# Kernel tuning notes

Measured on AMD Instinct MI355X. Metric: run time of the kernel, lower is better.

Reference implementation:

```python
import jax, jax.numpy as jnp
import numpy as np

N, E, D, R, H = 50000, 200000, 128, 4, 64

def setup_inputs() -> dict:
    key = jax.random.key(0)
    ks = jax.random.split(key, 12)
    s = 0.02
    return {
        'node_feature': jax.random.normal(ks[0], (N, D), dtype=jnp.float32),
        'edge_src': jax.random.randint(ks[1], (E,), 0, N, dtype=jnp.int32),
        'edge_dst': jax.random.randint(ks[2], (E,), 0, N, dtype=jnp.int32),
        'edge_type': jax.random.randint(ks[3], (E,), 0, R, dtype=jnp.int32),
        'Wr1': s * jax.random.normal(ks[4], (R, D, H), dtype=jnp.float32),
        'br1': jnp.zeros((R, H), dtype=jnp.float32),
        'Wr2': s * jax.random.normal(ks[5], (R, H, H), dtype=jnp.float32),
        'br2': jnp.zeros((R, H), dtype=jnp.float32),
        'Wr3': s * jax.random.normal(ks[6], (R, H, D), dtype=jnp.float32),
        'br3': jnp.zeros((R, D), dtype=jnp.float32),
        'Wn1': s * jax.random.normal(ks[7], ((R + 1) * D, H), dtype=jnp.float32),
        'bn1': jnp.zeros((H,), dtype=jnp.float32),
        'Wn2': s * jax.random.normal(ks[8], (H, H), dtype=jnp.float32),
        'bn2': jnp.zeros((H,), dtype=jnp.float32),
        'Wn3': s * jax.random.normal(ks[9], (H, D), dtype=jnp.float32),
        'bn3': jnp.zeros((D,), dtype=jnp.float32),
    }

def reference(node_feature, edge_src, edge_dst, edge_type,
              Wr1, br1, Wr2, br2, Wr3, br3,
              Wn1, bn1, Wn2, bn2, Wn3, bn3):
    n, d = node_feature.shape
    r = Wr1.shape[0]
    # gather source node features per edge  [E, D]
    x_src = node_feature[edge_src]
    # per-relation message MLP over all edges (masked below): relu hidden layers,
    # linear output, then outer relu as in message_function
    h = jax.nn.relu(jnp.einsum('ed,rdh->reh', x_src, Wr1) + br1[:, None, :])
    h = jax.nn.relu(jnp.einsum('reh,rhk->rek', h, Wr2) + br2[:, None, :])
    msg = jax.nn.relu(jnp.einsum('rek,rkd->red', h, Wr3) + br3[:, None, :])  # [R, E, D]
    # zero out edges not of this relation type (mirrors boolean masking)
    mask = (edge_type[None, :] == jnp.arange(r, dtype=edge_type.dtype)[:, None])
    msg = msg * mask[:, :, None].astype(msg.dtype)
    # scatter-sum messages into destination node slots  [R, N, D]
    agg = jax.vmap(lambda m: jax.ops.segment_sum(m, edge_dst, num_segments=n))(msg)
    # node_enc_input: [relu(node_feature), agg_0, ..., agg_{R-1}]  -> [N, (R+1)*D]
    node_in = jnp.concatenate(
        [jax.nn.relu(node_feature), agg.transpose(1, 0, 2).reshape(n, r * d)], axis=1)
    # node updater MLP
    h = jax.nn.relu(node_in @ Wn1 + bn1)
    h = jax.nn.relu(h @ Wn2 + bn2)
    return h @ Wn3 + bn3
```

## Files before the change

kernel.cpp:

```cpp
#include <hip/hip_runtime.h>

#define DD 128
#define HH 64
#define RR 4
#define NT 256
#define NNT 512
#define DGRID 512
#define DPART 128

typedef __attribute__((ext_vector_type(8))) __bf16 bf16x8;
typedef __attribute__((ext_vector_type(4))) __bf16 bf16x4;
typedef __attribute__((ext_vector_type(4))) float f32x4;

#define SK128 136
#define SK64  72
#define ABLK  2176

#define O_W1  0
#define O_W2  8704
#define O_W3  13312
#define O_WP  22528
#define O_ACT 31232
#define DSMEM_ELEMS 39936
#define N_W1  0
#define N_W2  8704
#define N_W3  13312
#define N_ACT 22528
#define NSMEM_ELEMS 39936

#define W1T_OFF 0
#define W2T_OFF 32768
#define W3T_OFF 49152
#define WPT_OFF 81920
#define WN1_OFF 114688
#define WN2_OFF 122880
#define WN3_OFF 126976
#define WT_TOTAL 135168

#define MFMA(a, b, c) __builtin_amdgcn_mfma_f32_16x16x32_bf16(a, b, c, 0, 0, 0)


template<int ROWS, int COLS, int STRIDE, int BLK>
__device__ __forceinline__ void stageRM(const __bf16* __restrict__ g, __bf16* s, int tid) {
    constexpr int CH = COLS / 8;
    constexpr int TOT = ROWS * CH;
    #pragma unroll
    for (int i = tid; i < TOT; i += BLK) {
        const int row = i / CH, c8 = i % CH;
        *(bf16x8*)(s + row * STRIDE + c8 * 8) = *(const bf16x8*)(g + row * COLS + c8 * 8);
    }
}

__global__ void k_prep_hist(const float* __restrict__ Wr1, const float* __restrict__ Wr2,
                            const float* __restrict__ Wr3, const float* __restrict__ Wn1,
                            const float* __restrict__ Wn2, const float* __restrict__ Wn3,
                            __bf16* __restrict__ wt,
                            const int* __restrict__ ed, int* __restrict__ dstCnt, int E) {
    int i = blockIdx.x * blockDim.x + threadIdx.x;
    if (i < E) atomicAdd(&dstCnt[ed[i]], 1);
    if (i < 32768) {
        int r = i >> 13, k = (i >> 6) & 127, n = i & 63;
        wt[W1T_OFF + r * 8192 + n * 128 + k] = (__bf16)Wr1[i];
    } else if (i < 49152) {
        int j = i - 32768; int r = j >> 12, k = (j >> 6) & 63, n = j & 63;
        wt[W2T_OFF + r * 4096 + n * 64 + k] = (__bf16)Wr2[j];
    } else if (i < 81920) {
        int j = i - 49152; int r = j >> 13, k = (j >> 7) & 63, n = j & 127;
        wt[W3T_OFF + r * 8192 + n * 64 + k] = (__bf16)Wr3[j];
    } else if (i < 122880) {
        int j = i - 81920; int row = j >> 6, n = j & 63;
        int s = row >> 7, k = row & 127;
        float v = Wn1[j];
        if (s == 0) wt[WN1_OFF + n * 128 + k] = (__bf16)v;
        else        wt[WPT_OFF + (s - 1) * 8192 + n * 128 + k] = (__bf16)v;
    } else if (i < 126976) {
        int j = i - 122880; int k = j >> 6, n = j & 63;
        wt[WN2_OFF + n * 64 + k] = (__bf16)Wn2[j];
    } else if (i < WT_TOTAL) {
        int j = i - 126976; int k = j >> 7, n = j & 127;
        wt[WN3_OFF + n * 64 + k] = (__bf16)Wn3[j];
    }
}

__global__ void k_bsum(const int* __restrict__ dstCnt, int* __restrict__ blkSum, int Nn) {
    int b = blockIdx.x, t = threadIdx.x;
    int g = b * 1024 + t * 4;
    int s = 0;
    if (g + 3 < Nn) { int4 v = *(const int4*)(dstCnt + g); s = v.x + v.y + v.z + v.w; }
    else { for (int k = 0; k < 4; k++) if (g + k < Nn) s += dstCnt[g + k]; }
    for (int off = 32; off > 0; off >>= 1) s += __shfl_down(s, off);
    __shared__ int ws[4];
    if ((t & 63) == 0) ws[t >> 6] = s;
    __syncthreads();
    if (t == 0) blkSum[b] = ws[0] + ws[1] + ws[2] + ws[3];
}

__global__ void k_mid(const int* __restrict__ blkSum, int* __restrict__ blkOff,
                      int* __restrict__ rowStart, int NB, int Nn, int E) {
    int lane = threadIdx.x;
    int s = (lane < NB) ? blkSum[lane] : 0;
    int sc = s;
    #pragma unroll
    for (int off = 1; off < 64; off <<= 1) { int u = __shfl_up(sc, off); if (lane >= off) sc += u; }
    if (lane < NB) blkOff[lane] = sc - s;
    if (lane == 0) rowStart[Nn] = E;
}

__global__ void k_wout(const int* __restrict__ dstCnt, const int* __restrict__ blkOff,
                       int* __restrict__ rowStart, int* __restrict__ dstCursor, int Nn) {
    int b = blockIdx.x, t = threadIdx.x;
    int g = b * 1024 + t * 4;
    int4 v = {0, 0, 0, 0};
    bool full = (g + 3 < Nn);
    if (full) v = *(const int4*)(dstCnt + g);
    else {
        if (g     < Nn) v.x = dstCnt[g];
        if (g + 1 < Nn) v.y = dstCnt[g + 1];
        if (g + 2 < Nn) v.z = dstCnt[g + 2];
    }
    int s = v.x + v.y + v.z + v.w;
    int lane = t & 63, wv = t >> 6;
    int sc = s;
    #pragma unroll
    for (int off = 1; off < 64; off <<= 1) { int u = __shfl_up(sc, off); if (lane >= off) sc += u; }
    __shared__ int wsum[4];
    if (lane == 63) wsum[wv] = sc;
    __syncthreads();
    int wadd = 0;
    for (int i = 0; i < wv; i++) wadd += wsum[i];
    int e0 = blkOff[b] + wadd + sc - s;
    int4 rs; rs.x = e0; rs.y = e0 + v.x; rs.z = rs.y + v.y; rs.w = rs.z + v.z;
    if (full) { *(int4*)(rowStart + g) = rs; *(int4*)(dstCursor + g) = rs; }
    else {
        int a[4] = {rs.x, rs.y, rs.z, rs.w};
        for (int k = 0; k < 4; k++) if (g + k < Nn) { rowStart[g + k] = a[k]; dstCursor[g + k] = a[k]; }
    }
}

__global__ void k_place(const int* __restrict__ et, const int* __restrict__ ed,
                        const int* __restrict__ es, int* __restrict__ dstCursor,
                        int* __restrict__ csrKey, int E, int Nn) {
    int i = blockIdx.x * blockDim.x + threadIdx.x;
    if (i < E) {
        int sl = atomicAdd(&dstCursor[ed[i]], 1);
        csrKey[sl] = et[i] * Nn + es[i];
    }
}

__global__ __launch_bounds__(NT, 2) void k_dense(
    const float* __restrict__ nf,
    const float* __restrict__ br1, const float* __restrict__ br2, const float* __restrict__ br3,
    const __bf16* __restrict__ wt, __bf16* __restrict__ ca, int Nn)
{
    extern __shared__ __bf16 smem[];
    const int r    = blockIdx.x & 3;
    const int part = blockIdx.x >> 2;
    const int tid  = threadIdx.x;
    const int w = tid >> 6;
    const int lane = tid & 63;
    const int ln = lane & 15, qd = lane >> 4;
    const int m0 = w << 4;
    __bf16* act = smem + O_ACT + w * ABLK;

    stageRM<64, 128, SK128, NT>(wt + W1T_OFF + r * 8192, smem + O_W1, tid);
    stageRM<64,  64, SK64 , NT>(wt + W2T_OFF + r * 4096, smem + O_W2, tid);
    stageRM<128, 64, SK64 , NT>(wt + W3T_OFF + r * 8192, smem + O_W3, tid);
    stageRM<64, 128, SK128, NT>(wt + WPT_OFF + r * 8192, smem + O_WP, tid);

    float bv1[4], bv2[4], bv3[8];
    #pragma unroll
    for (int nt = 0; nt < 4; nt++) {
        bv1[nt] = br1[r * HH + nt * 16 + ln];
        bv2[nt] = br2[r * HH + nt * 16 + ln];
    }
    #pragma unroll
    for (int nt = 0; nt < 8; nt++) bv3[nt] = br3[r * DD + nt * 16 + ln];

    const int T = (Nn + 63) >> 6;
    const int mx = tid >> 2, qx = tid & 3;
    __bf16* xr = act + (mx & 15) * SK128 + 32 * qx;

    float4 xv[8];
    int t = part;
    if (t < T) {
        const int node = min(t * 64 + mx, Nn - 1);
        const float4* rp = (const float4*)(nf + (size_t)node * DD) + 8 * qx;
        #pragma unroll
        for (int j = 0; j < 8; j++) xv[j] = rp[j];
    }
    __syncthreads();

    for (; t < T; t += DPART) {
        const int nb0 = t * 64;

        #pragma unroll
        for (int jj = 0; jj < 4; jj++) {
            float4 v0 = xv[2 * jj], v1 = xv[2 * jj + 1];
            bf16x8 p;
            p[0] = (__bf16)v0.x; p[1] = (__bf16)v0.y; p[2] = (__bf16)v0.z; p[3] = (__bf16)v0.w;
            p[4] = (__bf16)v1.x; p[5] = (__bf16)v1.y; p[6] = (__bf16)v1.z; p[7] = (__bf16)v1.w;
            *(bf16x8*)(xr + 8 * jj) = p;
        }
        bf16x8 ax[4];
        #pragma unroll
        for (int i = 0; i < 4; i++)
            ax[i] = *(const bf16x8*)(act + ln * SK128 + i * 32 + 8 * qd);

        const int tn = t + DPART;
        if (tn < T) {
            const int node = min(tn * 64 + mx, Nn - 1);
            const float4* rp = (const float4*)(nf + (size_t)node * DD) + 8 * qx;
            #pragma unroll
            for (int j = 0; j < 8; j++) xv[j] = rp[j];
        }

        {
            f32x4 c[4] = {};
            #pragma unroll
            for (int kk = 0; kk < 4; kk++)
                #pragma unroll
                for (int nt = 0; nt < 4; nt++) {
                    bf16x8 b = *(const bf16x8*)(smem + O_W1 + (nt * 16 + ln) * SK128 + kk * 32 + 8 * qd);
                    c[nt] = MFMA(ax[kk], b, c[nt]);
                }
            #pragma unroll
            for (int nt = 0; nt < 4; nt++)
                #pragma unroll
                for (int rg = 0; rg < 4; rg++) {
                    float v = c[nt][rg] + bv1[nt];
                    act[(qd * 4 + rg) * SK64 + nt * 16 + ln] = (__bf16)fmaxf(v, 0.f);
                }
        }
        {
            bf16x8 a0 = *(const bf16x8*)(act + ln * SK64 + 0 + 8 * qd);
            bf16x8 a1 = *(const bf16x8*)(act + ln * SK64 + 32 + 8 * qd);
            f32x4 c[4] = {};
            #pragma unroll
            for (int nt = 0; nt < 4; nt++) {
                bf16x8 b0 = *(const bf16x8*)(smem + O_W2 + (nt * 16 + ln) * SK64 + 0 + 8 * qd);
                bf16x8 b1 = *(const bf16x8*)(smem + O_W2 + (nt * 16 + ln) * SK64 + 32 + 8 * qd);
                c[nt] = MFMA(a0, b0, c[nt]);
                c[nt] = MFMA(a1, b1, c[nt]);
            }
            #pragma unroll
            for (int nt = 0; nt < 4; nt++)
                #pragma unroll
                for (int rg = 0; rg < 4; rg++) {
                    float v = c[nt][rg] + bv2[nt];
                    act[(qd * 4 + rg) * SK64 + nt * 16 + ln] = (__bf16)fmaxf(v, 0.f);
                }
        }
        {
            bf16x8 a0 = *(const bf16x8*)(act + ln * SK64 + 0 + 8 * qd);
            bf16x8 a1 = *(const bf16x8*)(act + ln * SK64 + 32 + 8 * qd);
            f32x4 c[8];
            #pragma unroll
            for (int nt = 0; nt < 8; nt++) {
                bf16x8 b0 = *(const bf16x8*)(smem + O_W3 + (nt * 16 + ln) * SK64 + 0 + 8 * qd);
                bf16x8 b1 = *(const bf16x8*)(smem + O_W3 + (nt * 16 + ln) * SK64 + 32 + 8 * qd);
                f32x4 acc = {};
                acc = MFMA(a0, b0, acc);
                acc = MFMA(a1, b1, acc);
                c[nt] = acc;
            }
            #pragma unroll
            for (int nt = 0; nt < 8; nt++)
                #pragma unroll
                for (int rg = 0; rg < 4; rg++) {
                    float v = c[nt][rg] + bv3[nt];
                    act[(qd * 4 + rg) * SK128 + nt * 16 + ln] = (__bf16)fmaxf(v, 0.f);
                }
        }
        {
            bf16x8 am[4];
            #pragma unroll
            for (int i = 0; i < 4; i++)
                am[i] = *(const bf16x8*)(act + ln * SK128 + i * 32 + 8 * qd);
            f32x4 c[4] = {};
            #pragma unroll
            for (int kk = 0; kk < 4; kk++)
                #pragma unroll
                for (int nt = 0; nt < 4; nt++) {
                    bf16x8 b = *(const bf16x8*)(smem + O_WP + (nt * 16 + ln) * SK128 + kk * 32 + 8 * qd);
                    c[nt] = MFMA(am[kk], b, c[nt]);
                }
            #pragma unroll
            for (int rg = 0; rg < 4; rg++) {
                const int node = nb0 + m0 + qd * 4 + rg;
                if (node < Nn) {
                    bf16x4 v;
                    v[0] = (__bf16)c[0][rg]; v[1] = (__bf16)c[1][rg];
                    v[2] = (__bf16)c[2][rg]; v[3] = (__bf16)c[3][rg];
                    *(bf16x4*)(ca + ((size_t)r * Nn + node) * HH + ln * 4) = v;
                }
            }
        }
    }
}

__global__ __launch_bounds__(NNT, 4) void k_node(
    const float* __restrict__ nf,
    const float* __restrict__ bn1, const float* __restrict__ bn2, const float* __restrict__ bn3,
    const __bf16* __restrict__ wt, const __bf16* __restrict__ ca,
    const int* __restrict__ rowStart, const int* __restrict__ csrKey,
    float* __restrict__ out, int Nn)
{
    extern __shared__ __bf16 smem[];
    const int nb0 = blockIdx.x * 128;
    const int tid = threadIdx.x;
    const int w = tid >> 6;
    const int lane = tid & 63;
    const int ln = lane & 15, qd = lane >> 4;
    const int m0 = w << 4;
    __bf16* act = smem + N_ACT + w * ABLK;

    stageRM<64, 128, SK128, NNT>(wt + WN1_OFF, smem + N_W1, tid);
    stageRM<64,  64, SK64 , NNT>(wt + WN2_OFF, smem + N_W2, tid);
    stageRM<128, 64, SK64 , NNT>(wt + WN3_OFF, smem + N_W3, tid);
    {
        const int m = tid >> 2, q = tid & 3;
        const int node = min(nb0 + m, Nn - 1);
        const float4* rp = (const float4*)(nf + (size_t)node * DD) + 8 * q;
        __bf16* xr = act + (m & 15) * SK128 + 32 * q;
        #pragma unroll
        for (int jj = 0; jj < 4; jj++) {
            float4 v0 = rp[2 * jj], v1 = rp[2 * jj + 1];
            bf16x8 p;
            p[0] = (__bf16)fmaxf(v0.x, 0.f); p[1] = (__bf16)fmaxf(v0.y, 0.f);
            p[2] = (__bf16)fmaxf(v0.z, 0.f); p[3] = (__bf16)fmaxf(v0.w, 0.f);
            p[4] = (__bf16)fmaxf(v1.x, 0.f); p[5] = (__bf16)fmaxf(v1.y, 0.f);
            p[6] = (__bf16)fmaxf(v1.z, 0.f); p[7] = (__bf16)fmaxf(v1.w, 0.f);
            *(bf16x8*)(xr + 8 * jj) = p;
        }
    }
    bf16x8 ax[4];
    #pragma unroll
    for (int i = 0; i < 4; i++)
        ax[i] = *(const bf16x8*)(act + ln * SK128 + i * 32 + 8 * qd);

    float bv1[4], bv2[4], bv3[8];
    #pragma unroll
    for (int nt = 0; nt < 4; nt++) { bv1[nt] = bn1[nt * 16 + ln]; bv2[nt] = bn2[nt * 16 + ln]; }
    #pragma unroll
    for (int nt = 0; nt < 8; nt++) bv3[nt] = bn3[nt * 16 + ln];

    float agg[4][4] = {};
    {
        const int base = nb0 + m0 + qd * 4;
        int rs[5];
        #pragma unroll
        for (int j = 0; j < 5; j++) rs[j] = rowStart[min(base + j, Nn)];
        int cur[4];
        #pragma unroll
        for (int rg = 0; rg < 4; rg++) cur[rg] = rs[rg];
        const __bf16* cab = ca + ln * 4;

        while (true) {
            int k0[4], k1[4];
            bool v0[4], v1[4];
            bool any = false;
            #pragma unroll
            for (int rg = 0; rg < 4; rg++) {
                const int c0 = cur[rg], e1 = rs[rg + 1];
                v0[rg] = c0 < e1;
                v1[rg] = c0 + 1 < e1;
                if (v0[rg]) k0[rg] = csrKey[c0];
                if (v1[rg]) k1[rg] = csrKey[c0 + 1];
                cur[rg] = c0 + (v0[rg] ? 1 : 0) + (v1[rg] ? 1 : 0);
                any |= v0[rg];
            }
            if (!any) break;
            #pragma unroll
            for (int rg = 0; rg < 4; rg++) {
                if (v0[rg]) {
                    const bf16x4 x = *(const bf16x4*)(cab + (size_t)k0[rg] * HH);
                    agg[rg][0] += (float)x[0]; agg[rg][1] += (float)x[1];
                    agg[rg][2] += (float)x[2]; agg[rg][3] += (float)x[3];
                }
                if (v1[rg]) {
                    const bf16x4 x = *(const bf16x4*)(cab + (size_t)k1[rg] * HH);
                    agg[rg][0] += (float)x[0]; agg[rg][1] += (float)x[1];
                    agg[rg][2] += (float)x[2]; agg[rg][3] += (float)x[3];
                }
            }
        }
    }
    __syncthreads();

    {
        f32x4 c[4] = {};
        #pragma unroll
        for (int kk = 0; kk < 4; kk++)
            #pragma unroll
            for (int nt = 0; nt < 4; nt++) {
                bf16x8 b = *(const bf16x8*)(smem + N_W1 + (nt * 16 + ln) * SK128 + kk * 32 + 8 * qd);
                c[nt] = MFMA(ax[kk], b, c[nt]);
            }
        #pragma unroll
        for (int nt = 0; nt < 4; nt++)
            #pragma unroll
            for (int rg = 0; rg < 4; rg++) {
                float v = c[nt][rg] + bv1[nt] + agg[rg][nt];
                act[(qd * 4 + rg) * SK64 + nt * 16 + ln] = (__bf16)fmaxf(v, 0.f);
            }
    }
    {
        bf16x8 a0 = *(const bf16x8*)(act + ln * SK64 + 0 + 8 * qd);
        bf16x8 a1 = *(const bf16x8*)(act + ln * SK64 + 32 + 8 * qd);
        f32x4 c[4] = {};
        #pragma unroll
        for (int nt = 0; nt < 4; nt++) {
            bf16x8 b0 = *(const bf16x8*)(smem + N_W2 + (nt * 16 + ln) * SK64 + 0 + 8 * qd);
            bf16x8 b1 = *(const bf16x8*)(smem + N_W2 + (nt * 16 + ln) * SK64 + 32 + 8 * qd);
            c[nt] = MFMA(a0, b0, c[nt]);
            c[nt] = MFMA(a1, b1, c[nt]);
        }
        #pragma unroll
        for (int nt = 0; nt < 4; nt++)
            #pragma unroll
            for (int rg = 0; rg < 4; rg++) {
                float v = c[nt][rg] + bv2[nt];
                act[(qd * 4 + rg) * SK64 + nt * 16 + ln] = (__bf16)fmaxf(v, 0.f);
            }
    }
    {
        bf16x8 a0 = *(const bf16x8*)(act + ln * SK64 + 0 + 8 * qd);
        bf16x8 a1 = *(const bf16x8*)(act + ln * SK64 + 32 + 8 * qd);
        f32x4 c[8];
        #pragma unroll
        for (int nt = 0; nt < 8; nt++) {
            bf16x8 b0 = *(const bf16x8*)(smem + N_W3 + (nt * 16 + ln) * SK64 + 0 + 8 * qd);
            bf16x8 b1 = *(const bf16x8*)(smem + N_W3 + (nt * 16 + ln) * SK64 + 32 + 8 * qd);
            f32x4 acc = {};
            acc = MFMA(a0, b0, acc);
            acc = MFMA(a1, b1, acc);
            c[nt] = acc;
        }
        #pragma unroll
        for (int rg = 0; rg < 4; rg++) {
            const int node = nb0 + m0 + qd * 4 + rg;
            if (node < Nn) {
                float* op = out + (size_t)node * DD;
                #pragma unroll
                for (int nt = 0; nt < 8; nt++)
                    op[nt * 16 + ln] = c[nt][rg] + bv3[nt];
            }
        }
    }
}

extern "C" void kernel_launch(void* const* d_in, const int* in_sizes, int n_in,
                              void* d_out, int out_size, void* d_ws, size_t ws_size,
                              hipStream_t stream) {
    const float* nf  = (const float*)d_in[0];
    const int*   es  = (const int*)d_in[1];
    const int*   ed  = (const int*)d_in[2];
    const int*   et  = (const int*)d_in[3];
    const float* Wr1 = (const float*)d_in[4];
    const float* br1 = (const float*)d_in[5];
    const float* Wr2 = (const float*)d_in[6];
    const float* br2 = (const float*)d_in[7];
    const float* Wr3 = (const float*)d_in[8];
    const float* br3 = (const float*)d_in[9];
    const float* Wn1 = (const float*)d_in[10];
    const float* bn1 = (const float*)d_in[11];
    const float* Wn2 = (const float*)d_in[12];
    const float* bn2 = (const float*)d_in[13];
    const float* Wn3 = (const float*)d_in[14];
    const float* bn3 = (const float*)d_in[15];
    float* out = (float*)d_out;

    const int Nn = in_sizes[0] / DD;
    const int E  = in_sizes[1];
    const int NB = (Nn + 1023) / 1024;

    int* p = (int*)d_ws;
    int* dstCnt    = p;                 p += Nn;
    int* dstCursor = p;                 p += Nn;
    int* rowStart  = p;                 p += Nn + 1;
    int* blkSum    = p;                 p += 64;
    int* blkOff    = p;                 p += 64;
    int* csrKey    = p;                 p += E;
    p += ((8 - ((p - (int*)d_ws) & 7)) & 7);
    __bf16* wbf = (__bf16*)p;           p += (WT_TOTAL + 1) / 2;
    __bf16* ca  = (__bf16*)p;

    hipFuncSetAttribute((const void*)k_dense,
                        hipFuncAttributeMaxDynamicSharedMemorySize,
                        DSMEM_ELEMS * (int)sizeof(__bf16));
    hipFuncSetAttribute((const void*)k_node,
                        hipFuncAttributeMaxDynamicSharedMemorySize,
                        NSMEM_ELEMS * (int)sizeof(__bf16));

    hipMemsetAsync((void*)dstCnt, 0, (size_t)Nn * sizeof(int), stream);

    const int nb = (E + NT - 1) / NT;
    k_prep_hist<<<nb, NT, 0, stream>>>(Wr1, Wr2, Wr3, Wn1, Wn2, Wn3, wbf, ed, dstCnt, E);
    k_bsum <<<NB, 256, 0, stream>>>(dstCnt, blkSum, Nn);
    k_mid  <<<1, 64, 0, stream>>>(blkSum, blkOff, rowStart, NB, Nn, E);
    k_wout <<<NB, 256, 0, stream>>>(dstCnt, blkOff, rowStart, dstCursor, Nn);
    k_place<<<nb, NT, 0, stream>>>(et, ed, es, dstCursor, csrKey, E, Nn);

    k_dense<<<DGRID, NT, DSMEM_ELEMS * sizeof(__bf16), stream>>>(nf, br1, br2, br3, wbf, ca, Nn);
    k_node <<<(Nn + 127) / 128, NNT, NSMEM_ELEMS * sizeof(__bf16), stream>>>(
        nf, bn1, bn2, bn3, wbf, ca, rowStart, csrKey, out, Nn);
}
```

Before: 183.4 us.

## Fuse CSR scan and edge placement into dense kernel via grid barrier

Removes the separate block-sum, mid-scan, write-out and placement kernels and performs the prefix scan and CSR placement inside the first NB blocks of k_dense, using an atomic spin grid barrier. The scheduling of dense tiles is reversed so the blocks doing CSR work get fewer or later tiles. This cuts four kernel launches and their gaps but relies on all NB blocks being co-resident for the spin barrier. It also serialises the placement atomics onto a small set of blocks (NB=49).

```diff
diff --git a/kernel.cpp b/kernel.cpp
--- a/kernel.cpp
+++ b/kernel.cpp
@@ -7,6 +7,7 @@
 #define NNT 512
 #define DGRID 512
 #define DPART 128
+#define MFMA(a, b, c) __builtin_amdgcn_mfma_f32_16x16x32_bf16(a, b, c, 0, 0, 0)
 
 typedef __attribute__((ext_vector_type(8))) __bf16 bf16x8;
 typedef __attribute__((ext_vector_type(4))) __bf16 bf16x4;
@@ -37,8 +38,17 @@
 #define WN3_OFF 126976
 #define WT_TOTAL 135168
 
-#define MFMA(a, b, c) __builtin_amdgcn_mfma_f32_16x16x32_bf16(a, b, c, 0, 0, 0)
-
+
+__device__ __forceinline__ void gbar(int* bar, int target) {
+    __syncthreads();
+    if (threadIdx.x == 0) {
+        __hip_atomic_fetch_add(bar, 1, __ATOMIC_RELEASE, __HIP_MEMORY_SCOPE_AGENT);
+        while (__hip_atomic_load(bar, __ATOMIC_RELAXED, __HIP_MEMORY_SCOPE_AGENT) < target)
+            __builtin_amdgcn_s_sleep(1);
+        __threadfence();
+    }
+    __syncthreads();
+}
 
 template<int ROWS, int COLS, int STRIDE, int BLK>
 __device__ __forceinline__ void stageRM(const __bf16* __restrict__ g, __bf16* s, int tid) {
@@ -82,80 +92,20 @@
     }
 }
 
-__global__ void k_bsum(const int* __restrict__ dstCnt, int* __restrict__ blkSum, int Nn) {
-    int b = blockIdx.x, t = threadIdx.x;
-    int g = b * 1024 + t * 4;
-    int s = 0;
-    if (g + 3 < Nn) { int4 v = *(const int4*)(dstCnt + g); s = v.x + v.y + v.z + v.w; }
-    else { for (int k = 0; k < 4; k++) if (g + k < Nn) s += dstCnt[g + k]; }
-    for (int off = 32; off > 0; off >>= 1) s += __shfl_down(s, off);
-    __shared__ int ws[4];
-    if ((t & 63) == 0) ws[t >> 6] = s;
-    __syncthreads();
-    if (t == 0) blkSum[b] = ws[0] + ws[1] + ws[2] + ws[3];
-}
-
-__global__ void k_mid(const int* __restrict__ blkSum, int* __restrict__ blkOff,
-                      int* __restrict__ rowStart, int NB, int Nn, int E) {
-    int lane = threadIdx.x;
-    int s = (lane < NB) ? blkSum[lane] : 0;
-    int sc = s;
-    #pragma unroll
-    for (int off = 1; off < 64; off <<= 1) { int u = __shfl_up(sc, off); if (lane >= off) sc += u; }
-    if (lane < NB) blkOff[lane] = sc - s;
-    if (lane == 0) rowStart[Nn] = E;
-}
-
-__global__ void k_wout(const int* __restrict__ dstCnt, const int* __restrict__ blkOff,
-                       int* __restrict__ rowStart, int* __restrict__ dstCursor, int Nn) {
-    int b = blockIdx.x, t = threadIdx.x;
-    int g = b * 1024 + t * 4;
-    int4 v = {0, 0, 0, 0};
-    bool full = (g + 3 < Nn);
-    if (full) v = *(const int4*)(dstCnt + g);
-    else {
-        if (g     < Nn) v.x = dstCnt[g];
-        if (g + 1 < Nn) v.y = dstCnt[g + 1];
-        if (g + 2 < Nn) v.z = dstCnt[g + 2];
-    }
-    int s = v.x + v.y + v.z + v.w;
-    int lane = t & 63, wv = t >> 6;
-    int sc = s;
-    #pragma unroll
-    for (int off = 1; off < 64; off <<= 1) { int u = __shfl_up(sc, off); if (lane >= off) sc += u; }
-    __shared__ int wsum[4];
-    if (lane == 63) wsum[wv] = sc;
-    __syncthreads();
-    int wadd = 0;
-    for (int i = 0; i < wv; i++) wadd += wsum[i];
-    int e0 = blkOff[b] + wadd + sc - s;
-    int4 rs; rs.x = e0; rs.y = e0 + v.x; rs.z = rs.y + v.y; rs.w = rs.z + v.z;
-    if (full) { *(int4*)(rowStart + g) = rs; *(int4*)(dstCursor + g) = rs; }
-    else {
-        int a[4] = {rs.x, rs.y, rs.z, rs.w};
-        for (int k = 0; k < 4; k++) if (g + k < Nn) { rowStart[g + k] = a[k]; dstCursor[g + k] = a[k]; }
-    }
-}
-
-__global__ void k_place(const int* __restrict__ et, const int* __restrict__ ed,
-                        const int* __restrict__ es, int* __restrict__ dstCursor,
-                        int* __restrict__ csrKey, int E, int Nn) {
-    int i = blockIdx.x * blockDim.x + threadIdx.x;
-    if (i < E) {
-        int sl = atomicAdd(&dstCursor[ed[i]], 1);
-        csrKey[sl] = et[i] * Nn + es[i];
-    }
-}
-
 __global__ __launch_bounds__(NT, 2) void k_dense(
     const float* __restrict__ nf,
+    const int* __restrict__ es, const int* __restrict__ ed, const int* __restrict__ et,
     const float* __restrict__ br1, const float* __restrict__ br2, const float* __restrict__ br3,
-    const __bf16* __restrict__ wt, __bf16* __restrict__ ca, int Nn)
+    const __bf16* __restrict__ wt, __bf16* __restrict__ ca,
+    int* bar, const int* __restrict__ dstCnt, int* dstCursor,
+    int* __restrict__ rowStart, int* blkSum, int* __restrict__ csrKey,
+    int Nn, int E, int NB)
 {
     extern __shared__ __bf16 smem[];
-    const int r    = blockIdx.x & 3;
-    const int part = blockIdx.x >> 2;
-    const int tid  = threadIdx.x;
+    const int bid = blockIdx.x;
+    const int r   = bid & 3;
+    const int part = (DPART - 1) - (bid >> 2);
+    const int tid = threadIdx.x;
     const int w = tid >> 6;
     const int lane = tid & 63;
     const int ln = lane & 15, qd = lane >> 4;
@@ -167,6 +117,56 @@
     stageRM<128, 64, SK64 , NT>(wt + W3T_OFF + r * 8192, smem + O_W3, tid);
     stageRM<64, 128, SK128, NT>(wt + WPT_OFF + r * 8192, smem + O_WP, tid);
 
+    if (bid < NB) {
+        int* iw = (int*)(smem + O_ACT);
+        const int g = bid * 1024 + tid * 4;
+        int4 v = {0, 0, 0, 0};
+        const bool full = (g + 3 < Nn);
+        if (full) v = *(const int4*)(dstCnt + g);
+        else {
+            if (g     < Nn) v.x = dstCnt[g];
+            if (g + 1 < Nn) v.y = dstCnt[g + 1];
+            if (g + 2 < Nn) v.z = dstCnt[g + 2];
+        }
+        const int s = v.x + v.y + v.z + v.w;
+        int sc = s;
+        #pragma unroll
+        for (int off = 1; off < 64; off <<= 1) { int u = __shfl_up(sc, off); if (lane >= off) sc += u; }
+        if (lane == 63) iw[w] = sc;
+        __syncthreads();
+        int wadd = 0;
+        for (int i = 0; i < w; i++) wadd += iw[i];
+        if (tid == 0) blkSum[bid] = iw[0] + iw[1] + iw[2] + iw[3];
+        gbar(bar, NB);
+        if (tid < 64) {
+            int sb = (tid < NB) ? blkSum[tid] : 0;
+            int scb = sb;
+            #pragma unroll
+            for (int off = 1; off < 64; off <<= 1) { int u = __shfl_up(scb, off); if (tid >= off) scb += u; }
+            int ex = __shfl(scb, bid > 0 ? bid - 1 : 0);
+            if (tid == 0) iw[8] = (bid > 0) ? ex : 0;
+        }
+        __syncthreads();
+        const int e0 = iw[8] + wadd + sc - s;
+        int4 rs; rs.x = e0; rs.y = e0 + v.x; rs.z = rs.y + v.y; rs.w = rs.z + v.z;
+        if (full) {
+            *(int4*)(rowStart + g) = rs;
+            *(int4*)(dstCursor + g) = rs;
+        } else {
+            int a[4] = {rs.x, rs.y, rs.z, rs.w};
+            for (int k = 0; k < 4; k++) if (g + k < Nn) {
+                rowStart[g + k] = a[k];
+                dstCursor[g + k] = a[k];
+            }
+        }
+        if (bid == 0 && tid == 0) rowStart[Nn] = E;
+        gbar(bar, 2 * NB);
+        for (int i = bid * NT + tid; i < E; i += NB * NT) {
+            int sl = atomicAdd(&dstCursor[ed[i]], 1);
+            csrKey[sl] = et[i] * Nn + es[i];
+        }
+    }
+
     float bv1[4], bv2[4], bv3[8];
     #pragma unroll
     for (int nt = 0; nt < 4; nt++) {
@@ -180,8 +180,8 @@
     const int mx = tid >> 2, qx = tid & 3;
     __bf16* xr = act + (mx & 15) * SK128 + 32 * qx;
 
+    int t = part;
     float4 xv[8];
-    int t = part;
     if (t < T) {
         const int node = min(t * 64 + mx, Nn - 1);
         const float4* rp = (const float4*)(nf + (size_t)node * DD) + 8 * qx;
@@ -192,7 +192,6 @@
 
     for (; t < T; t += DPART) {
         const int nb0 = t * 64;
-
         #pragma unroll
         for (int jj = 0; jj < 4; jj++) {
             float4 v0 = xv[2 * jj], v1 = xv[2 * jj + 1];
@@ -288,10 +287,10 @@
             for (int rg = 0; rg < 4; rg++) {
                 const int node = nb0 + m0 + qd * 4 + rg;
                 if (node < Nn) {
-                    bf16x4 v;
-                    v[0] = (__bf16)c[0][rg]; v[1] = (__bf16)c[1][rg];
-                    v[2] = (__bf16)c[2][rg]; v[3] = (__bf16)c[3][rg];
-                    *(bf16x4*)(ca + ((size_t)r * Nn + node) * HH + ln * 4) = v;
+                    bf16x4 vv;
+                    vv[0] = (__bf16)c[0][rg]; vv[1] = (__bf16)c[1][rg];
+                    vv[2] = (__bf16)c[2][rg]; vv[3] = (__bf16)c[3][rg];
+                    *(bf16x4*)(ca + ((size_t)r * Nn + node) * HH + ln * 4) = vv;
                 }
             }
         }
@@ -470,16 +469,16 @@
     const float* bn3 = (const float*)d_in[15];
     float* out = (float*)d_out;
 
-    const int Nn = in_sizes[0] / DD;
-    const int E  = in_sizes[1];
-    const int NB = (Nn + 1023) / 1024;
+    int Nn = in_sizes[0] / DD;
+    int E  = in_sizes[1];
+    int NB = (Nn + 1023) / 1024;
 
     int* p = (int*)d_ws;
+    int* bar       = p;                 p += 4;
     int* dstCnt    = p;                 p += Nn;
     int* dstCursor = p;                 p += Nn;
     int* rowStart  = p;                 p += Nn + 1;
     int* blkSum    = p;                 p += 64;
-    int* blkOff    = p;                 p += 64;
     int* csrKey    = p;                 p += E;
     p += ((8 - ((p - (int*)d_ws) & 7)) & 7);
     __bf16* wbf = (__bf16*)p;           p += (WT_TOTAL + 1) / 2;
@@ -492,16 +491,15 @@
                         hipFuncAttributeMaxDynamicSharedMemorySize,
                         NSMEM_ELEMS * (int)sizeof(__bf16));
 
-    hipMemsetAsync((void*)dstCnt, 0, (size_t)Nn * sizeof(int), stream);
+    hipMemsetAsync(d_ws, 0, (size_t)(4 + Nn) * sizeof(int), stream);
 
     const int nb = (E + NT - 1) / NT;
     k_prep_hist<<<nb, NT, 0, stream>>>(Wr1, Wr2, Wr3, Wn1, Wn2, Wn3, wbf, ed, dstCnt, E);
-    k_bsum <<<NB, 256, 0, stream>>>(dstCnt, blkSum, Nn);
-    k_mid  <<<1, 64, 0, stream>>>(blkSum, blkOff, rowStart, NB, Nn, E);
-    k_wout <<<NB, 256, 0, stream>>>(dstCnt, blkOff, rowStart, dstCursor, Nn);
-    k_place<<<nb, NT, 0, stream>>>(et, ed, es, dstCursor, csrKey, E, Nn);
-
-    k_dense<<<DGRID, NT, DSMEM_ELEMS * sizeof(__bf16), stream>>>(nf, br1, br2, br3, wbf, ca, Nn);
-    k_node <<<(Nn + 127) / 128, NNT, NSMEM_ELEMS * sizeof(__bf16), stream>>>(
+
+    k_dense<<<DGRID, NT, DSMEM_ELEMS * sizeof(__bf16), stream>>>(
+        nf, es, ed, et, br1, br2, br3, wbf, ca,
+        bar, dstCnt, dstCursor, rowStart, blkSum, csrKey, Nn, E, NB);
+
+    k_node<<<(Nn + 127) / 128, NNT, NSMEM_ELEMS * sizeof(__bf16), stream>>>(
         nf, bn1, bn2, bn3, wbf, ca, rowStart, csrKey, out, Nn);
 }
```

Measured after the change: 193.4 us. 1.05x slower.
